# Kernel optimization log

Hardware: AMD Instinct MI355X
Metric: run time of the kernel (lower is better)

The kernel has to match this reference:

```python
import jax, jax.numpy as jnp
import numpy as np

# Module constants (from init_kwargs + mp_num=8 from the mesh)
D_MODEL = 1024
N_HEAD = 16
D_HEAD = 64
D_ROT = 64
MP = 8
B, S = 2, 2048
LOCAL = N_HEAD * D_HEAD // MP          # 128 : per-mp-shard qkv dim
F_IN = N_HEAD * D_HEAD * 3 + D_MODEL * 8  # 11264 : fused qkv+ff projection width
D_OUT_IN = D_MODEL + 4 * D_MODEL       # 5120 : attn (1024) + glu (4096) into output_proj
LN_EPS = 1e-5


def _rotate_every_two(x):
    # x: [..., d] with d even -> interleaved (-x2, x1)
    x1 = x[..., ::2]
    x2 = x[..., 1::2]
    return jnp.stack((-x2, x1), axis=-1).reshape(*x.shape[:-1], -1)


def _fixed_pos_embedding(seq_len, dim):
    inv_freq = 1.0 / (10000.0 ** (np.arange(0, dim, 2) / dim))
    t = np.einsum('i,j->ij', np.arange(seq_len), inv_freq)  # [S, dim//2]
    return jnp.asarray(np.sin(t), jnp.float32), jnp.asarray(np.cos(t), jnp.float32)


def _apply_rotary(x, sin, cos):
    # x: [B, S, mp, D_ROT]; sin/cos: [S, D_ROT//2]
    sin = jnp.repeat(sin, 2, axis=-1)[-x.shape[-3]:, None, :]  # [S,1,D_ROT]
    cos = jnp.repeat(cos, 2, axis=-1)[-x.shape[-3]:, None, :]
    return x * cos + _rotate_every_two(x) * sin


def setup_inputs() -> dict:
    key = jax.random.key(0)
    ks = jax.random.split(key, 4)
    x = jax.random.normal(ks[0], (B, S, D_MODEL), jnp.float32)
    attn_bias = jnp.zeros((1, S, S), jnp.float32)
    ln_scale = jnp.ones((D_MODEL,), jnp.float32)
    ln_offset = jnp.zeros((D_MODEL,), jnp.float32)
    w_in = jax.random.normal(ks[1], (D_MODEL, F_IN), jnp.float32) / np.sqrt(D_MODEL)
    b_in = jnp.zeros((F_IN,), jnp.float32)
    w_out = jax.random.normal(ks[2], (D_OUT_IN, D_MODEL), jnp.float32) / np.sqrt(D_MODEL)
    b_out = jnp.zeros((D_MODEL,), jnp.float32)
    return {"x": x, "attn_bias": attn_bias, "ln_scale": ln_scale, "ln_offset": ln_offset,
            "w_in": w_in, "b_in": b_in, "w_out": w_out, "b_out": b_out}


def reference(x, attn_bias, ln_scale, ln_offset, w_in, b_in, w_out, b_out):
    b, s, d = x.shape
    # LayerNorm (create_scale=True, create_offset=True, eps=1e-5)
    mu = jnp.mean(x, axis=-1, keepdims=True)
    var = jnp.var(x, axis=-1, keepdims=True)
    h = (x - mu) * jax.lax.rsqrt(var + LN_EPS) * ln_scale + ln_offset
    # fused QKV + FF projection, then mp split: [B,S,mp,F_IN/mp]
    proj = (h @ w_in + b_in).reshape(b, s, MP, -1)
    q, v, k, ff = jnp.split(proj, [LOCAL, 2 * LOCAL, 3 * LOCAL], axis=-1)
    # rotary on the first D_ROT dims of each mp shard (head_split is a shape no-op)
    sin, cos = _fixed_pos_embedding(s, D_ROT)
    q = jnp.concatenate([_apply_rotary(q[..., :D_ROT], sin, cos), q[..., D_ROT:]], axis=-1)
    k = jnp.concatenate([_apply_rotary(k[..., :D_ROT], sin, cos), k[..., D_ROT:]], axis=-1)
    # attention over h=mp shard-heads of dim LOCAL; scaled by sqrt(d_head) per source
    scale = np.sqrt(D_HEAD).astype(x.dtype)
    logits = jnp.einsum('bthd,bThd->bhtT', q, k) / scale  # [B,MP,S,S]
    causal = jnp.tril(jnp.ones((s, s), x.dtype))[None]
    bias = -1e10 * (1.0 - causal) + attn_bias
    weights = jax.nn.softmax(logits + bias, axis=-1)
    attn_vec = jnp.einsum('bhtT,bThd->bthd', weights, v)  # [B,S,MP,LOCAL]
    # GLU FFN (jax.nn.gelu default = tanh approximation, as in source)
    ff_out, ff_gate = jnp.split(ff, 2, axis=-1)
    glu = ff_out * jax.nn.gelu(ff_gate)  # [B,S,MP,4*D_MODEL/MP]
    # output: concat per-shard then flatten -> output_proj
    out = jnp.concatenate([attn_vec, glu], axis=-1).reshape(b, s, -1)  # [B,S,5120]
    return out @ w_out + b_out
```

## Files before the change

### kernel.cpp

```cpp
#include <hip/hip_runtime.h>
#include <stdint.h>

#define B_   2
#define S_   2048
#define DM   1024
#define FIN  11264
#define DOUT 5120
#define NSH  8
#define DH   128
#define ROWS (B_*S_)

typedef __attribute__((ext_vector_type(8))) __bf16 bf16x8;
typedef __attribute__((ext_vector_type(4))) __bf16 bf16x4;
typedef __attribute__((ext_vector_type(4))) float  f32x4;

union U2 { unsigned int u; __bf16 h[2]; };

__device__ __forceinline__ void gload16(const void* g, void* l) {
    __builtin_amdgcn_global_load_lds((const __attribute__((address_space(1))) void*)g,
                                     (__attribute__((address_space(3))) void*)l, 16, 0, 0);
}

__device__ __forceinline__ int origcol(int c) {
    if (c < 3072) { int p = c / 384; return p*1408 + (c - p*384); }
    int q = c - 3072; int p = q >> 10; int w = q & 1023;
    int a = w >> 5, g = (w >> 4) & 1, u = w & 15;
    return p*1408 + 384 + g*512 + a*16 + u;
}

__global__ __launch_bounds__(256) void ln_kernel(const float* __restrict__ x,
                                                 const float* __restrict__ sc,
                                                 const float* __restrict__ of,
                                                 __bf16* __restrict__ h) {
    int row = blockIdx.x, t = threadIdx.x;
    const float4 v = *(const float4*)&x[(size_t)row*DM + t*4];
    float s  = v.x + v.y + v.z + v.w;
    float ss = v.x*v.x + v.y*v.y + v.z*v.z + v.w*v.w;
#pragma unroll
    for (int off = 32; off >= 1; off >>= 1) {
        s  += __shfl_xor(s, off);
        ss += __shfl_xor(ss, off);
    }
    __shared__ float rs_[4], rss_[4];
    int wid = t >> 6, lane = t & 63;
    if (lane == 0) { rs_[wid] = s; rss_[wid] = ss; }
    __syncthreads();
    s  = rs_[0] + rs_[1] + rs_[2] + rs_[3];
    ss = rss_[0] + rss_[1] + rss_[2] + rss_[3];
    float mu  = s * (1.f/DM);
    float var = ss * (1.f/DM) - mu*mu;
    float r   = rsqrtf(var + 1e-5f);
    float4 scv = *(const float4*)&sc[t*4];
    float4 ofv = *(const float4*)&of[t*4];
    bf16x4 o;
    o[0] = (__bf16)((v.x-mu)*r*scv.x + ofv.x);
    o[1] = (__bf16)((v.y-mu)*r*scv.y + ofv.y);
    o[2] = (__bf16)((v.z-mu)*r*scv.z + ofv.z);
    o[3] = (__bf16)((v.w-mu)*r*scv.w + ofv.w);
    *(bf16x4*)&h[(size_t)row*DM + t*4] = o;
}

__global__ __launch_bounds__(256) void transpose_kernel(const float* __restrict__ in,
                                                        __bf16* __restrict__ out,
                                                        int R, int C) {
    __shared__ __bf16 tile[64][72];
    int c0 = blockIdx.x * 64, r0 = blockIdx.y * 64;
    int t = threadIdx.x;
#pragma unroll
    for (int it = 0; it < 4; ++it) {
        int flat = it*1024 + t*4;
        int rl = flat >> 6, cl = flat & 63;
        float4 v = *(const float4*)&in[(size_t)(r0+rl)*C + c0 + cl];
        tile[rl][cl+0] = (__bf16)v.x;
        tile[rl][cl+1] = (__bf16)v.y;
        tile[rl][cl+2] = (__bf16)v.z;
        tile[rl][cl+3] = (__bf16)v.w;
    }
    __syncthreads();
#pragma unroll
    for (int it = 0; it < 4; ++it) {
        int flat = it*1024 + t*4;
        int cl = flat >> 6, rl = flat & 63;
        bf16x4 o;
#pragma unroll
        for (int j = 0; j < 4; ++j) o[j] = tile[rl+j][cl];
        *(bf16x4*)&out[(size_t)(c0+cl)*R + r0 + rl] = o;
    }
}

__global__ __launch_bounds__(256) void transpose_perm_kernel(const float* __restrict__ in,
                                                             __bf16* __restrict__ out) {
    __shared__ __bf16 tile[64][72];
    int c0 = blockIdx.x * 64, r0 = blockIdx.y * 64;
    int t = threadIdx.x;
#pragma unroll
    for (int it = 0; it < 4; ++it) {
        int flat = it*1024 + t*4;
        int rl = flat >> 6, cl = flat & 63;
        int oc = origcol(c0 + cl);
        float4 v = *(const float4*)&in[(size_t)(r0+rl)*FIN + oc];
        tile[rl][cl+0] = (__bf16)v.x;
        tile[rl][cl+1] = (__bf16)v.y;
        tile[rl][cl+2] = (__bf16)v.z;
        tile[rl][cl+3] = (__bf16)v.w;
    }
    __syncthreads();
#pragma unroll
    for (int it = 0; it < 4; ++it) {
        int flat = it*1024 + t*4;
        int cl = flat >> 6, rl = flat & 63;
        bf16x4 o;
#pragma unroll
        for (int j = 0; j < 4; ++j) o[j] = tile[rl+j][cl];
        *(bf16x4*)&out[(size_t)(c0+cl)*DM + r0 + rl] = o;
    }
}

__global__ __launch_bounds__(256) void permbias_kernel(const float* __restrict__ b_in,
                                                       float* __restrict__ bp) {
    int c = blockIdx.x * 256 + threadIdx.x;
    if (c < FIN) bp[c] = b_in[origcol(c)];
}

#define MFMA4(ACCI, BN) \
    acc[ACCI][BN] = __builtin_amdgcn_mfma_f32_16x16x32_bf16(a[(ACCI)&3][0], b[BN][0], acc[ACCI][BN],0,0,0); \
    acc[ACCI][BN] = __builtin_amdgcn_mfma_f32_16x16x32_bf16(a[(ACCI)&3][1], b[BN][1], acc[ACCI][BN],0,0,0);

__global__ __launch_bounds__(512, 2) void gemm1_kernel(const __bf16* __restrict__ A,
                                                       const __bf16* __restrict__ BT,
                                                       const float* __restrict__ bias,
                                                       __bf16* __restrict__ Cqvk,
                                                       __bf16* __restrict__ Cglu) {
    const int M = ROWS, N = FIN, K = DM;
    __shared__ __align__(16) char lds[131072];
    int t = threadIdx.x, wid = t >> 6, lane = t & 63;
    int wr = wid >> 2, wc = wid & 3;
    int fr = lane & 15, fq = lane >> 4;
    int nbx = gridDim.x;
    int bid = blockIdx.y * nbx + blockIdx.x;
    int cpx = (nbx * gridDim.y) >> 3;
    int swz = (bid & 7) * cpx + (bid >> 3);
    int bx = swz % nbx, by = swz / nbx;
    int m0 = by * 256, n0 = bx * 256;

    const __bf16* srcA[4];
    const __bf16* srcB[4];
#pragma unroll
    for (int j = 0; j < 4; ++j) {
        int F = (j*512 + t) * 16;
        int lr = F >> 7, c = (F & 127) ^ ((lr & 7) << 4);
        srcA[j] = A + (size_t)(m0 + lr) * K + (c >> 1);
        int row = ((lr >> 5) & 3) * 64 + (lr >> 7) * 32 + (lr & 31);
        srcB[j] = BT + (size_t)(n0 + row) * K + (c >> 1);
    }
    int lrAlo[4], lrAhi[4], lrB[4];
#pragma unroll
    for (int i = 0; i < 4; ++i) {
        lrAlo[i] = (wr*128 + i*16 + fr) * 128;
        lrAhi[i] = lrAlo[i] + 64*128;
    }
#pragma unroll
    for (int n = 0; n < 4; ++n)
        lrB[n] = ((n >> 1)*128 + wc*32 + (n & 1)*16 + fr) * 128;
    int swzb = (fr & 7) << 4;
    int cb00 = (fq*16) ^ swzb;
    int cb01 = (64 + fq*16) ^ swzb;

    f32x4 acc[8][4] = {};
    gload16(srcA[0], lds +     0 + wid*1024);
    gload16(srcA[2], lds + 16384 + wid*1024);
    gload16(srcB[0], lds + 32768 + wid*1024);
    gload16(srcB[1], lds + 40960 + wid*1024);
    gload16(srcB[2], lds + 49152 + wid*1024);
    gload16(srcB[3], lds + 57344 + wid*1024);
    gload16(srcA[1], lds +  8192 + wid*1024);
    gload16(srcA[3], lds + 24576 + wid*1024);
    asm volatile("s_waitcnt vmcnt(4)" ::: "memory");
    __builtin_amdgcn_s_barrier();

    int nit = K >> 6;
    for (int it = 0; it < nit; ++it) {
        const char* bc = lds + (it & 1) * 65536;
        char* bn = lds + ((it & 1) ^ 1) * 65536;
        const char* bcB = bc + 32768;
        int koff = (it + 1) << 6;
        bool pf = (it + 1 < nit);
        bf16x8 a[4][2], b[4][2];
#pragma unroll
        for (int i = 0; i < 4; ++i) {
            a[i][0] = *(const bf16x8*)(bc + lrAlo[i] + cb00);
            a[i][1] = *(const bf16x8*)(bc + lrAlo[i] + cb01);
        }
        b[0][0] = *(const bf16x8*)(bcB + lrB[0] + cb00);
        b[0][1] = *(const bf16x8*)(bcB + lrB[0] + cb01);
        b[1][0] = *(const bf16x8*)(bcB + lrB[1] + cb00);
        b[1][1] = *(const bf16x8*)(bcB + lrB[1] + cb01);
        if (pf) {
            gload16(srcA[0] + koff, bn +     0 + wid*1024);
            gload16(srcA[2] + koff, bn + 16384 + wid*1024);
            gload16(srcB[0] + koff, bn + 32768 + wid*1024);
            gload16(srcB[1] + koff, bn + 40960 + wid*1024);
            gload16(srcB[2] + koff, bn + 49152 + wid*1024);
            gload16(srcB[3] + koff, bn + 57344 + wid*1024);
            gload16(srcA[1] + koff, bn +  8192 + wid*1024);
            gload16(srcA[3] + koff, bn + 24576 + wid*1024);
        }
        __builtin_amdgcn_s_setprio(1);
#pragma unroll
        for (int i = 0; i < 4; ++i) { MFMA4(i,0) MFMA4(i,1) }
        __builtin_amdgcn_s_setprio(0);
        if (pf) asm volatile("s_waitcnt vmcnt(10)" ::: "memory");
        else    asm volatile("s_waitcnt vmcnt(2)" ::: "memory");
        __builtin_amdgcn_s_barrier();
        b[2][0] = *(const bf16x8*)(bcB + lrB[2] + cb00);
        b[2][1] = *(const bf16x8*)(bcB + lrB[2] + cb01);
        b[3][0] = *(const bf16x8*)(bcB + lrB[3] + cb00);
        b[3][1] = *(const bf16x8*)(bcB + lrB[3] + cb01);
        __builtin_amdgcn_s_setprio(1);
#pragma unroll
        for (int i = 0; i < 4; ++i) { MFMA4(i,2) MFMA4(i,3) }
        __builtin_amdgcn_s_setprio(0);
        if (pf) asm volatile("s_waitcnt vmcnt(8)" ::: "memory");
        else    asm volatile("s_waitcnt vmcnt(0)" ::: "memory");
        __builtin_amdgcn_s_barrier();
#pragma unroll
        for (int i = 0; i < 4; ++i) {
            a[i][0] = *(const bf16x8*)(bc + lrAhi[i] + cb00);
            a[i][1] = *(const bf16x8*)(bc + lrAhi[i] + cb01);
        }
        __builtin_amdgcn_s_setprio(1);
#pragma unroll
        for (int i = 0; i < 4; ++i) { MFMA4(4+i,0) MFMA4(4+i,1) MFMA4(4+i,2) MFMA4(4+i,3) }
        __builtin_amdgcn_s_setprio(0);
        if (pf) {
            asm volatile("s_waitcnt vmcnt(4)" ::: "memory");
            __builtin_amdgcn_s_barrier();
        }
    }
    if (n0 < 3072) {
#pragma unroll
        for (int i = 0; i < 8; ++i)
#pragma unroll
            for (int n = 0; n < 4; ++n) {
                int col = n0 + wc*64 + (n >> 1)*32 + (n & 1)*16 + fr;
                float bv = bias[col];
#pragma unroll
                for (int r = 0; r < 4; ++r) {
                    int row = m0 + wr*128 + i*16 + fq*4 + r;
                    Cqvk[(size_t)row*3072 + col] = (__bf16)(acc[i][n][r] + bv);
                }
            }
    } else {
        int q = n0 - 3072;
        int p = q >> 10;
#pragma unroll
        for (int m = 0; m < 2; ++m) {
            int off = wc*64 + m*32;
            float bo = bias[n0 + off + fr];
            float bg = bias[n0 + off + 16 + fr];
            int j = (((q & 1023) + off) >> 5) * 16 + fr;
            int colg = p*640 + 128 + j;
#pragma unroll
            for (int i = 0; i < 8; ++i)
#pragma unroll
                for (int r = 0; r < 4; ++r) {
                    int row = m0 + wr*128 + i*16 + fq*4 + r;
                    float ov = acc[i][2*m][r] + bo;
                    float gv = acc[i][2*m+1][r] + bg;
                    float e2 = __expf(1.5957691216057308f*(gv + 0.044715f*gv*gv*gv));
                    float gl = gv * (1.f - 1.f/(e2 + 1.f));
                    Cglu[(size_t)row*DOUT + colg] = (__bf16)(ov * gl);
                }
        }
    }
}

__global__ __launch_bounds__(256, 4) void gemm2_kernel(const __bf16* __restrict__ A,
                                                       const __bf16* __restrict__ BT,
                                                       float* __restrict__ P,
                                                       int klen) {
    const int M = ROWS, N = DM, K = DOUT;
    __shared__ __align__(16) char lds[32768];
    int t = threadIdx.x, wid = t >> 6, lane = t & 63;
    int wm = (wid >> 1) * 64, wn = (wid & 1) * 64;
    int fr = lane & 15, fq = lane >> 4;
    int kbeg = blockIdx.z * klen;
    int nbx = gridDim.x;
    int bid = blockIdx.y * nbx + blockIdx.x;
    int cpx = (nbx * gridDim.y) >> 3;
    int swz = (bid & 7) * cpx + (bid >> 3);
    int bx = swz % nbx, by = swz / nbx;
    int m0 = by * 128, n0 = bx * 128;

    const __bf16* srcA[4];
    const __bf16* srcB[4];
#pragma unroll
    for (int j = 0; j < 4; ++j) {
        int F = (j*256 + t) * 16;
        int row = F >> 7;
        int c = (F & 127) ^ ((row & 7) << 4);
        srcA[j] = A  + (size_t)(m0 + row) * K + kbeg + (c >> 1);
        srcB[j] = BT + (size_t)(n0 + row) * K + kbeg + (c >> 1);
    }
    int rowA[4], rowB[4];
#pragma unroll
    for (int i = 0; i < 4; ++i) {
        rowA[i] = (wm + i*16 + fr) * 128;
        rowB[i] = 16384 + (wn + i*16 + fr) * 128;
    }
    int swzb = (fr & 7) << 4;
    int cb0 = (fq*16) ^ swzb;
    int cb1 = (64 + fq*16) ^ swzb;

    f32x4 acc[4][4] = {};
    for (int k0 = 0; k0 < klen; k0 += 64) {
#pragma unroll
        for (int j = 0; j < 4; ++j)
            gload16(srcA[j] + k0, lds + j*4096 + wid*1024);
#pragma unroll
        for (int j = 0; j < 4; ++j)
            gload16(srcB[j] + k0, lds + 16384 + j*4096 + wid*1024);
        __syncthreads();
        bf16x8 a[4], b[4];
#pragma unroll
        for (int i = 0; i < 4; ++i) a[i] = *(const bf16x8*)(lds + rowA[i] + cb0);
#pragma unroll
        for (int n = 0; n < 4; ++n) b[n] = *(const bf16x8*)(lds + rowB[n] + cb0);
#pragma unroll
        for (int i = 0; i < 4; ++i)
#pragma unroll
            for (int n = 0; n < 4; ++n)
                acc[i][n] = __builtin_amdgcn_mfma_f32_16x16x32_bf16(a[i], b[n], acc[i][n], 0, 0, 0);
#pragma unroll
        for (int i = 0; i < 4; ++i) a[i] = *(const bf16x8*)(lds + rowA[i] + cb1);
#pragma unroll
        for (int n = 0; n < 4; ++n) b[n] = *(const bf16x8*)(lds + rowB[n] + cb1);
#pragma unroll
        for (int i = 0; i < 4; ++i)
#pragma unroll
            for (int n = 0; n < 4; ++n)
                acc[i][n] = __builtin_amdgcn_mfma_f32_16x16x32_bf16(a[i], b[n], acc[i][n], 0, 0, 0);
        __syncthreads();
    }
    float* Pz = P + (size_t)blockIdx.z * M * N;
#pragma unroll
    for (int i = 0; i < 4; ++i)
#pragma unroll
        for (int n = 0; n < 4; ++n) {
            int col = n0 + wn + n*16 + fr;
#pragma unroll
            for (int r = 0; r < 4; ++r) {
                int row = m0 + wm + i*16 + fq*4 + r;
                Pz[(size_t)row*N + col] = acc[i][n][r];
            }
        }
}

__global__ __launch_bounds__(256) void addbias2_kernel(const float* __restrict__ pk,
                                                       const float* __restrict__ bias,
                                                       float* __restrict__ out) {
    int idx = blockIdx.x * 256 + threadIdx.x;
    const size_t stride = (size_t)ROWS * DM / 4;
    float4 a0 = ((const float4*)pk)[idx];
    float4 a1 = ((const float4*)pk)[idx + stride];
    float4 bb = ((const float4*)bias)[idx & 255];
    float4 o;
    o.x = a0.x + a1.x + bb.x;
    o.y = a0.y + a1.y + bb.y;
    o.z = a0.z + a1.z + bb.z;
    o.w = a0.w + a1.w + bb.w;
    ((float4*)out)[idx] = o;
}

__global__ __launch_bounds__(256) void rqkv_kernel(const __bf16* __restrict__ proj2,
                                                   __bf16* __restrict__ qh,
                                                   __bf16* __restrict__ kh,
                                                   __bf16* __restrict__ vt) {
    __shared__ __bf16 tile[64*144];
    int r0 = blockIdx.x * 64;
    int p  = blockIdx.y;
    int t  = threadIdx.x;
    int b  = r0 >> 11;
    int bh = b*NSH + p;
#pragma unroll
    for (int j = 0; j < 4; ++j) {
        int e = (j*256 + t) * 8;
        int sl = e >> 7, d = e & 127;
        const __bf16* rowp = proj2 + (size_t)(r0 + sl)*3072 + p*384;
        bf16x8 vq = *(const bf16x8*)&rowp[d];
        bf16x8 vv = *(const bf16x8*)&rowp[128 + d];
        bf16x8 vk = *(const bf16x8*)&rowp[256 + d];
        int s = (r0 + sl) & (S_ - 1);
        if (d < 64) {
#pragma unroll
            for (int u = 0; u < 4; ++u) {
                int i = (d >> 1) + u;
                float inv = exp2f(-(float)i * 0.4152410118609203f);
                float ang = (float)s * inv;
                float cn = __cosf(ang), sn = __sinf(ang);
                float q0 = vq[2*u], q1 = vq[2*u+1];
                float k0 = vk[2*u], k1 = vk[2*u+1];
                vq[2*u]   = (__bf16)(q0*cn - q1*sn);
                vq[2*u+1] = (__bf16)(q1*cn + q0*sn);
                vk[2*u]   = (__bf16)(k0*cn - k1*sn);
                vk[2*u+1] = (__bf16)(k1*cn + k0*sn);
            }
        }
#pragma unroll
        for (int u = 0; u < 8; ++u) vq[u] = (__bf16)((float)vq[u] * 0.125f);
        size_t o = ((size_t)bh * S_ + s) * DH + d;
        *(bf16x8*)&qh[o] = vq;
        *(bf16x8*)&kh[o] = vk;
        int ch = ((d >> 3) + sl) & 15;
        *(bf16x8*)&tile[sl*144 + ch*8] = vv;
    }
    __syncthreads();
#pragma unroll
    for (int j = 0; j < 4; ++j) {
        int e = (j*256 + t) * 8;
        int d = e >> 6, sb = e & 63;
        bf16x8 o;
#pragma unroll
        for (int u = 0; u < 8; ++u) {
            int sl = sb + u;
            int ch = ((d >> 3) + sl) & 15;
            o[u] = tile[sl*144 + ch*8 + (d & 7)];
        }
        size_t ov = ((size_t)bh * DH + d) * S_ + (r0 & (S_ - 1)) + sb;
        *(bf16x8*)&vt[ov] = o;
    }
}

__device__ __forceinline__ void stage_kv(const __bf16* Kb, const __bf16* Vg,
                                         char* KsB, char* VsB,
                                         int kvbase, int t, int wid) {
#pragma unroll
    for (int j = 0; j < 4; ++j) {
        int F = (j*256 + t)*16;
        int r = F >> 8, c = F & 255;
        gload16(Kb + (size_t)(kvbase + r)*DH + ((c ^ ((r & 7) << 4)) >> 1),
                KsB + j*4096 + (wid << 10));
    }
#pragma unroll
    for (int j = 0; j < 4; ++j) {
        int F = (j*256 + t)*16;
        int r = F >> 7, c = F & 127;
        gload16(Vg + (size_t)r*S_ + kvbase + ((c ^ ((r & 7) << 4)) >> 1),
                VsB + j*4096 + (wid << 10));
    }
}

__global__ __launch_bounds__(256, 2) void attn_kernel(const __bf16* __restrict__ qh,
                                                      const __bf16* __restrict__ kh,
                                                      const __bf16* __restrict__ vt,
                                                      const float* __restrict__ ab,
                                                      __bf16* __restrict__ ag) {
    __shared__ __bf16 Ks[2*8192];
    __shared__ __bf16 Vs[2*8192];
    __shared__ __bf16 Ps[4][16*72];
    int bh = blockIdx.y;
    int b = bh >> 3, hh = bh & 7;
    int xr = blockIdx.x;
    int qb = (xr & 1) ? (31 - (xr >> 1)) : (xr >> 1);
    int q0 = qb * 64;
    int t = threadIdx.x, wid = t >> 6, lane = t & 63;
    int fr = lane & 15, fkb = (lane >> 4) * 16;
    const __bf16* Qb = qh + (size_t)bh * S_ * DH;
    const __bf16* Kb = kh + (size_t)bh * S_ * DH;
    const __bf16* Vg = vt + (size_t)bh * DH * S_;
    bf16x8 qf[4];
#pragma unroll
    for (int kk = 0; kk < 4; ++kk)
        qf[kk] = *(const bf16x8*)&Qb[(size_t)(q0 + wid*16 + fr)*DH + kk*32 + (lane>>4)*8];
    float m[4] = {-3e38f, -3e38f, -3e38f, -3e38f};
    float l[4] = {0.f, 0.f, 0.f, 0.f};
    f32x4 o[8] = {};
    int rowb = q0 + wid*16 + (lane >> 4)*4;
    int nit = qb + 1;
    stage_kv(Kb, Vg, (char*)Ks, (char*)Vs, 0, t, wid);
    for (int it = 0; it < nit; ++it) {
        int kv0 = it * 64, cur = it & 1;
        float abv[4][4];
#pragma unroll
        for (int n = 0; n < 4; ++n)
#pragma unroll
            for (int r = 0; r < 4; ++r)
                abv[n][r] = ab[(size_t)(rowb + r)*S_ + kv0 + n*16 + fr];
        if (it + 1 < nit) {
            stage_kv(Kb, Vg, (char*)Ks + (cur^1)*16384, (char*)Vs + (cur^1)*16384,
                     kv0 + 64, t, wid);
            asm volatile("s_waitcnt vmcnt(8)" ::: "memory");
        } else {
            asm volatile("s_waitcnt vmcnt(0)" ::: "memory");
        }
        __builtin_amdgcn_s_barrier();
        const char* KsC = (const char*)Ks + cur*16384;
        float pv[4][4];
        __builtin_amdgcn_s_setprio(1);
#pragma unroll
        for (int n = 0; n < 4; ++n) {
            f32x4 sacc = {};
#pragma unroll
            for (int kk = 0; kk < 4; ++kk) {
                int row = n*16 + fr;
                int c2 = (kk*64 + fkb) ^ ((fr & 7) << 4);
                bf16x8 kf = *(const bf16x8*)(KsC + row*256 + c2);
                sacc = __builtin_amdgcn_mfma_f32_16x16x32_bf16(qf[kk], kf, sacc, 0, 0, 0);
            }
#pragma unroll
            for (int r = 0; r < 4; ++r) pv[n][r] = sacc[r];
        }
        __builtin_amdgcn_s_setprio(0);
#pragma unroll
        for (int n = 0; n < 4; ++n) {
            int col = kv0 + n*16 + fr;
#pragma unroll
            for (int r = 0; r < 4; ++r)
                pv[n][r] += abv[n][r] + (col <= rowb + r ? 0.f : -1e10f);
        }
        float alpha[4];
#pragma unroll
        for (int r = 0; r < 4; ++r) {
            float mx = fmaxf(fmaxf(pv[0][r], pv[1][r]), fmaxf(pv[2][r], pv[3][r]));
#pragma unroll
            for (int off = 8; off >= 1; off >>= 1) mx = fmaxf(mx, __shfl_xor(mx, off));
            float mn = fmaxf(m[r], mx);
            alpha[r] = __expf(m[r] - mn);
            m[r] = mn;
            float sum = 0.f;
#pragma unroll
            for (int n = 0; n < 4; ++n) { pv[n][r] = __expf(pv[n][r] - mn); sum += pv[n][r]; }
#pragma unroll
            for (int off = 8; off >= 1; off >>= 1) sum += __shfl_xor(sum, off);
            l[r] = l[r]*alpha[r] + sum;
        }
#pragma unroll
        for (int nf = 0; nf < 8; ++nf)
#pragma unroll
            for (int r = 0; r < 4; ++r) o[nf][r] *= alpha[r];
#pragma unroll
        for (int n = 0; n < 4; ++n)
#pragma unroll
            for (int r = 0; r < 4; ++r)
                Ps[wid][((lane >> 4)*4 + r)*72 + n*16 + fr] = (__bf16)pv[n][r];
        asm volatile("s_waitcnt lgkmcnt(0)" ::: "memory");
        __builtin_amdgcn_sched_barrier(0);
        bf16x8 pf[2];
#pragma unroll
        for (int kk = 0; kk < 2; ++kk)
            pf[kk] = *(const bf16x8*)&Ps[wid][fr*72 + kk*32 + (lane>>4)*8];
        const char* VsC = (const char*)Vs + cur*16384;
        __builtin_amdgcn_s_setprio(1);
#pragma unroll
        for (int nf = 0; nf < 8; ++nf) {
#pragma unroll
            for (int kk = 0; kk < 2; ++kk) {
                int row = nf*16 + fr;
                int c2 = (kk*64 + fkb) ^ ((fr & 7) << 4);
                bf16x8 vf = *(const bf16x8*)(VsC + row*128 + c2);
                o[nf] = __builtin_amdgcn_mfma_f32_16x16x32_bf16(pf[kk], vf, o[nf], 0, 0, 0);
            }
        }
        __builtin_amdgcn_s_setprio(0);
        asm volatile("s_waitcnt lgkmcnt(0)" ::: "memory");
        __builtin_amdgcn_sched_barrier(0);
        __builtin_amdgcn_s_barrier();
    }
    int rq = (lane >> 4) * 4;
#pragma unroll
    for (int r = 0; r < 4; ++r) {
        float inv = 1.f / l[r];
#pragma unroll
        for (int nf = 0; nf < 8; ++nf) {
            int qr = q0 + wid*16 + rq + r;
            int d = nf*16 + fr;
            ag[((size_t)(b*S_ + qr))*DOUT + hh*640 + d] = (__bf16)(o[nf][r] * inv);
        }
    }
}

extern "C" void kernel_launch(void* const* d_in, const int* in_sizes, int n_in,
                              void* d_out, int out_size, void* d_ws, size_t ws_size,
                              hipStream_t stream) {
    const float* x     = (const float*)d_in[0];
    const float* ab    = (const float*)d_in[1];
    const float* lns   = (const float*)d_in[2];
    const float* lno   = (const float*)d_in[3];
    const float* w_in  = (const float*)d_in[4];
    const float* b_in  = (const float*)d_in[5];
    const float* w_out = (const float*)d_in[6];
    const float* b_out = (const float*)d_in[7];
    float* out = (float*)d_out;
    char* ws = (char*)d_ws;

    __bf16* w_in_t  = (__bf16*)(ws);
    __bf16* w_out_t = (__bf16*)(ws +  23068672);
    __bf16* hbuf    = (__bf16*)(ws +  33554432);
    __bf16* proj2   = (__bf16*)(ws +  41943040);
    __bf16* vtb     = (__bf16*)(ws +  67108864);
    __bf16* qh      = (__bf16*)(ws +  75497472);
    __bf16* kh      = (__bf16*)(ws +  83886080);
    __bf16* agb     = (__bf16*)(ws +  92274688);
    float*  pk      = (float*)(ws + 134217728);
    float*  bperm   = (float*)(ws + 167772160);

    transpose_perm_kernel<<<dim3(FIN/64, DM/64), 256, 0, stream>>>(w_in, w_in_t);
    transpose_kernel<<<dim3(DM/64, DOUT/64), 256, 0, stream>>>(w_out, w_out_t, DOUT, DM);
    permbias_kernel<<<(FIN + 255)/256, 256, 0, stream>>>(b_in, bperm);
    ln_kernel<<<ROWS, 256, 0, stream>>>(x, lns, lno, hbuf);
    gemm1_kernel<<<dim3(FIN/256, ROWS/256), 512, 0, stream>>>(hbuf, w_in_t, bperm,
                                                              proj2, agb);
    rqkv_kernel<<<dim3(ROWS/64, NSH), 256, 0, stream>>>(proj2, qh, kh, vtb);
    attn_kernel<<<dim3(S_/64, B_*NSH), 256, 0, stream>>>(qh, kh, vtb, ab, agb);
    gemm2_kernel<<<dim3(DM/128, ROWS/128, 2), 256, 0, stream>>>(agb, w_out_t, pk, DOUT/2);
    addbias2_kernel<<<ROWS*DM/1024, 256, 0, stream>>>(pk, b_out, out);
}
```

Measured before the change: 287.2 us.

## Split output GEMM K four ways with bf16 partials and raise attention occupancy

The output projection GEMM now splits K into four slices instead of two, producing 1024 blocks for more parallelism. Its partial sums are stored as bf16 rather than fp32, which halves partial-buffer traffic. The reduction kernel sums four bf16 partials plus bias. The attention kernel's launch bounds ask for 3 blocks per CU, which may force register spills, and bf16 partials lose some accuracy in the final sum.

```diff
diff --git a/kernel.cpp b/kernel.cpp
--- a/kernel.cpp
+++ b/kernel.cpp
@@ -277,7 +277,7 @@
 
 __global__ __launch_bounds__(256, 4) void gemm2_kernel(const __bf16* __restrict__ A,
                                                        const __bf16* __restrict__ BT,
-                                                       float* __restrict__ P,
+                                                       __bf16* __restrict__ P,
                                                        int klen) {
     const int M = ROWS, N = DM, K = DOUT;
     __shared__ __align__(16) char lds[32768];
@@ -342,7 +342,7 @@
                 acc[i][n] = __builtin_amdgcn_mfma_f32_16x16x32_bf16(a[i], b[n], acc[i][n], 0, 0, 0);
         __syncthreads();
     }
-    float* Pz = P + (size_t)blockIdx.z * M * N;
+    __bf16* Pz = P + (size_t)blockIdx.z * M * N;
 #pragma unroll
     for (int i = 0; i < 4; ++i)
 #pragma unroll
@@ -351,25 +351,24 @@
 #pragma unroll
             for (int r = 0; r < 4; ++r) {
                 int row = m0 + wm + i*16 + fq*4 + r;
-                Pz[(size_t)row*N + col] = acc[i][n][r];
+                Pz[(size_t)row*N + col] = (__bf16)acc[i][n][r];
             }
         }
 }
 
-__global__ __launch_bounds__(256) void addbias2_kernel(const float* __restrict__ pk,
+__global__ __launch_bounds__(256) void addbias4_kernel(const __bf16* __restrict__ pk,
                                                        const float* __restrict__ bias,
                                                        float* __restrict__ out) {
     int idx = blockIdx.x * 256 + threadIdx.x;
     const size_t stride = (size_t)ROWS * DM / 4;
-    float4 a0 = ((const float4*)pk)[idx];
-    float4 a1 = ((const float4*)pk)[idx + stride];
-    float4 bb = ((const float4*)bias)[idx & 255];
-    float4 o;
-    o.x = a0.x + a1.x + bb.x;
-    o.y = a0.y + a1.y + bb.y;
-    o.z = a0.z + a1.z + bb.z;
-    o.w = a0.w + a1.w + bb.w;
-    ((float4*)out)[idx] = o;
+    float4 s = ((const float4*)bias)[idx & 255];
+#pragma unroll
+    for (int z = 0; z < 4; ++z) {
+        bf16x4 v = ((const bf16x4*)pk)[idx + z*stride];
+        s.x += (float)v[0]; s.y += (float)v[1];
+        s.z += (float)v[2]; s.w += (float)v[3];
+    }
+    ((float4*)out)[idx] = s;
 }
 
 __global__ __launch_bounds__(256) void rqkv_kernel(const __bf16* __restrict__ proj2,
@@ -450,7 +449,7 @@
     }
 }
 
-__global__ __launch_bounds__(256, 2) void attn_kernel(const __bf16* __restrict__ qh,
+__global__ __launch_bounds__(256, 3) void attn_kernel(const __bf16* __restrict__ qh,
                                                       const __bf16* __restrict__ kh,
                                                       const __bf16* __restrict__ vt,
                                                       const float* __restrict__ ab,
@@ -601,7 +600,7 @@
     __bf16* qh      = (__bf16*)(ws +  75497472);
     __bf16* kh      = (__bf16*)(ws +  83886080);
     __bf16* agb     = (__bf16*)(ws +  92274688);
-    float*  pk      = (float*)(ws + 134217728);
+    __bf16* pkb     = (__bf16*)(ws + 134217728);
     float*  bperm   = (float*)(ws + 167772160);
 
     transpose_perm_kernel<<<dim3(FIN/64, DM/64), 256, 0, stream>>>(w_in, w_in_t);
@@ -612,6 +611,6 @@
                                                               proj2, agb);
     rqkv_kernel<<<dim3(ROWS/64, NSH), 256, 0, stream>>>(proj2, qh, kh, vtb);
     attn_kernel<<<dim3(S_/64, B_*NSH), 256, 0, stream>>>(qh, kh, vtb, ab, agb);
-    gemm2_kernel<<<dim3(DM/128, ROWS/128, 2), 256, 0, stream>>>(agb, w_out_t, pk, DOUT/2);
-    addbias2_kernel<<<ROWS*DM/1024, 256, 0, stream>>>(pk, b_out, out);
-}
+    gemm2_kernel<<<dim3(DM/128, ROWS/128, 4), 256, 0, stream>>>(agb, w_out_t, pkb, DOUT/4);
+    addbias4_kernel<<<ROWS*DM/1024, 256, 0, stream>>>(pkb, b_out, out);
+}
```

Result: slower. 295.7 us (+3.0%).
